# Optimization experiments

Hardware: AMD Instinct MI355X
Metric: run time of the kernel (lower is better)

The kernel has to match this reference:

```python
import jax, jax.numpy as jnp
import numpy as np
import math

N_EMBD = 2048
NUM_SLOTS = 32

def setup_inputs() -> dict:
    key = jax.random.key(0)
    ks = jax.random.split(key, 6)
    B, S, D = 4, 4096, N_EMBD
    x = jax.random.normal(ks[0], (B, S, D), dtype=jnp.float32)
    memory = jax.random.normal(ks[1], (1, NUM_SLOTS, D), dtype=jnp.float32)
    # nn.Linear weights stored as [out, in]; init scale ~ U(-1/sqrt(in), 1/sqrt(in))
    lim = 1.0 / math.sqrt(D)
    Wq = jax.random.uniform(ks[2], (D, D), minval=-lim, maxval=lim, dtype=jnp.float32)
    bq = jax.random.uniform(ks[3], (D,), minval=-lim, maxval=lim, dtype=jnp.float32)
    Wm = jax.random.uniform(ks[4], (D, D), minval=-lim, maxval=lim, dtype=jnp.float32)
    bm = jax.random.uniform(ks[5], (D,), minval=-lim, maxval=lim, dtype=jnp.float32)
    return {"x": x, "memory": memory, "Wq": Wq, "bq": bq, "Wm": Wm, "bm": bm}

def reference(x, memory, Wq, bq, Wm, bm):
    # query = x @ Wq^T + bq                         [B,S,D]
    query = jnp.einsum('bsd,ed->bse', x, Wq) + bq
    mem = memory[0]                                  # [M,D], M=32
    scale = 1.0 / math.sqrt(mem.shape[-1])
    attn = jnp.einsum('bsd,md->bsm', query, mem) * scale   # [B,S,M]
    w = jax.nn.softmax(attn, axis=-1)
    mem_out = jnp.einsum('bsm,md->bsd', w, mem)      # [B,S,D]
    mem_out = jnp.einsum('bsd,ed->bse', mem_out, Wm) + bm
    return x + mem_out
```

## Files before the change

kernel.cpp:

```cpp
#include <hip/hip_runtime.h>
#include <math.h>

#define D 2048
#define M 32
#define SCALE 0.022097086912079608f


__global__ __launch_bounds__(256) void k_wqmt(const float* __restrict__ Wq,
                                              const float* __restrict__ mem,
                                              float* __restrict__ WqmT) {
    __shared__ float memL[M * 128];
    const int t  = threadIdx.x;
    const int dc = blockIdx.x;
    const int ec = blockIdx.y;
    const int d  = dc * 256 + t;
    {
        const float4* mg = (const float4*)mem;
        float4* ml = (float4*)memL;
#pragma unroll
        for (int q = 0; q < 4; ++q) {
            int i4 = t + 256 * q;
            int m = i4 >> 5, c4 = i4 & 31;
            ml[i4] = mg[m * 512 + ec * 32 + c4];
        }
    }
    __syncthreads();
    float acc[M];
#pragma unroll
    for (int m = 0; m < M; ++m) acc[m] = 0.f;
    const float4* ml4 = (const float4*)memL;
    for (int ee = 0; ee < 128; ee += 4) {
        float q0 = Wq[(ec * 128 + ee + 0) * D + d];
        float q1 = Wq[(ec * 128 + ee + 1) * D + d];
        float q2 = Wq[(ec * 128 + ee + 2) * D + d];
        float q3 = Wq[(ec * 128 + ee + 3) * D + d];
#pragma unroll
        for (int m = 0; m < M; ++m) {
            float4 mv = ml4[m * 32 + (ee >> 2)];
            acc[m] = fmaf(q0, mv.x, fmaf(q1, mv.y, fmaf(q2, mv.z, fmaf(q3, mv.w, acc[m]))));
        }
    }
#pragma unroll
    for (int m = 0; m < M; ++m) atomicAdd(&WqmT[m * D + d], acc[m] * SCALE);
}

__global__ __launch_bounds__(256) void k_wm2(const float* __restrict__ Wm,
                                             const float* __restrict__ mem,
                                             float* __restrict__ Wm2) {
    __shared__ float tile[64 * 65];
    __shared__ float memL[M * 64];
    const int t  = threadIdx.x;
    const int et = blockIdx.x;
    const int dq = blockIdx.y;
    const int e0 = et * 64;
    const int el = t & 63, mg = t >> 6;
    float acc[8];
#pragma unroll
    for (int j = 0; j < 8; ++j) acc[j] = 0.f;
    for (int ds = 0; ds < 8; ++ds) {
        const int d0 = dq * 512 + ds * 64;
#pragma unroll
        for (int q = 0; q < 4; ++q) {
            int i  = (t >> 4) + 16 * q;
            int c4 = t & 15;
            float4 v = *(const float4*)&Wm[(e0 + i) * D + d0 + 4 * c4];
            tile[i * 65 + 4 * c4 + 0] = v.x;
            tile[i * 65 + 4 * c4 + 1] = v.y;
            tile[i * 65 + 4 * c4 + 2] = v.z;
            tile[i * 65 + 4 * c4 + 3] = v.w;
        }
#pragma unroll
        for (int q = 0; q < 2; ++q) {
            int i4 = t + 256 * q;
            int m = i4 >> 4, c4 = i4 & 15;
            *(float4*)&memL[m * 64 + 4 * c4] = *(const float4*)&mem[m * D + d0 + 4 * c4];
        }
        __syncthreads();
        const float4* ml4 = (const float4*)memL;
        for (int dd = 0; dd < 64; dd += 4) {
            float t0 = tile[el * 65 + dd + 0];
            float t1 = tile[el * 65 + dd + 1];
            float t2 = tile[el * 65 + dd + 2];
            float t3 = tile[el * 65 + dd + 3];
#pragma unroll
            for (int j = 0; j < 8; ++j) {
                float4 mv = ml4[(mg * 8 + j) * 16 + (dd >> 2)];
                acc[j] = fmaf(t0, mv.x, fmaf(t1, mv.y, fmaf(t2, mv.z, fmaf(t3, mv.w, acc[j]))));
            }
        }
        __syncthreads();
    }
#pragma unroll
    for (int j = 0; j < 8; ++j) atomicAdd(&Wm2[(mg * 8 + j) * D + e0 + el], acc[j]);
}

__global__ __launch_bounds__(256) void k_cq(const float* __restrict__ bq,
                                            const float* __restrict__ mem,
                                            float* __restrict__ cqs) {
    __shared__ float red[256 * 32];
    const int t = threadIdx.x;
    float acc[M];
#pragma unroll
    for (int m = 0; m < M; ++m) acc[m] = 0.f;
    for (int e = t; e < D; e += 256) {
        float b = bq[e];
#pragma unroll
        for (int m = 0; m < M; ++m) acc[m] = fmaf(b, mem[m * D + e], acc[m]);
    }
#pragma unroll
    for (int m = 0; m < M; ++m) red[t * 32 + m] = acc[m];
    __syncthreads();
    if (t < 32) {
        float s = 0.f;
        for (int i = 0; i < 256; ++i) s += red[i * 32 + t];
        cqs[t] = s * SCALE;
    }
}

__global__ __launch_bounds__(256, 2) void k_main(const float* __restrict__ x,
                                                 const float* __restrict__ WqmT,
                                                 const float* __restrict__ Wm2,
                                                 const float* __restrict__ cqs,
                                                 const float* __restrict__ bm,
                                                 float* __restrict__ out) {
    __shared__ float4 ldsW[M * 64];
    const int t    = threadIdx.x;
    const int wv   = t >> 6;
    const int lane = t & 63;
    const long row0 = (long)blockIdx.x * 8 + wv * 2;
    const float4* x40 = (const float4*)(x + row0 * D);
    const float4* x41 = (const float4*)(x + (row0 + 1) * D);
    float4 xr0[8], xr1[8];
#pragma unroll
    for (int j = 0; j < 8; ++j) { xr0[j] = x40[lane + 64 * j]; xr1[j] = x41[lane + 64 * j]; }

    float acc0[M], acc1[M];
#pragma unroll
    for (int m = 0; m < M; ++m) { acc0[m] = 0.f; acc1[m] = 0.f; }

    const float4* Wg = (const float4*)WqmT;
#pragma unroll
    for (int c = 0; c < 8; ++c) {
        {
            const int m = t >> 3, b4 = t & 7;
#pragma unroll
            for (int i = 0; i < 8; ++i)
                ldsW[m * 64 + b4 + 8 * i] = Wg[m * 512 + c * 64 + b4 + 8 * i];
        }
        __syncthreads();
        const float4 xa = xr0[c], xb = xr1[c];
#pragma unroll
        for (int m = 0; m < M; ++m) {
            float4 v = ldsW[m * 64 + lane];
            acc0[m] = fmaf(xa.x, v.x, fmaf(xa.y, v.y, fmaf(xa.z, v.z, fmaf(xa.w, v.w, acc0[m]))));
            acc1[m] = fmaf(xb.x, v.x, fmaf(xb.y, v.y, fmaf(xb.z, v.z, fmaf(xb.w, v.w, acc1[m]))));
        }
        __syncthreads();
    }

    float at0 = 0.f, at1 = 0.f;
#pragma unroll
    for (int m = 0; m < M; ++m) {
        float a0 = acc0[m], a1 = acc1[m];
#pragma unroll
        for (int s = 1; s < 64; s <<= 1) {
            a0 += __shfl_xor(a0, s, 64);
            a1 += __shfl_xor(a1, s, 64);
        }
        if ((lane & 31) == m) { at0 = a0; at1 = a1; }
    }
    const float cq = cqs[lane & 31];
    at0 += cq; at1 += cq;

    float mx0 = at0, mx1 = at1;
#pragma unroll
    for (int s = 1; s < 32; s <<= 1) {
        mx0 = fmaxf(mx0, __shfl_xor(mx0, s, 32));
        mx1 = fmaxf(mx1, __shfl_xor(mx1, s, 32));
    }
    float e0 = expf(at0 - mx0), e1 = expf(at1 - mx1);
    float s0 = e0, s1 = e1;
#pragma unroll
    for (int s = 1; s < 32; s <<= 1) {
        s0 += __shfl_xor(s0, s, 32);
        s1 += __shfl_xor(s1, s, 32);
    }
    const float w0 = e0 / s0, w1 = e1 / s1;

    const float4* W2g  = (const float4*)Wm2;
    const float4* bm4p = (const float4*)bm;
    float* o0p = out + row0 * D;
    float* o1p = out + (row0 + 1) * D;
#pragma unroll
    for (int c = 0; c < 8; ++c) {
        {
            const int m = t >> 3, b4 = t & 7;
#pragma unroll
            for (int i = 0; i < 8; ++i)
                ldsW[m * 64 + b4 + 8 * i] = W2g[m * 512 + c * 64 + b4 + 8 * i];
        }
        __syncthreads();
        float4 bmv = bm4p[lane + 64 * c];
        float4 o0 = xr0[c], o1 = xr1[c];
        o0.x += bmv.x; o0.y += bmv.y; o0.z += bmv.z; o0.w += bmv.w;
        o1.x += bmv.x; o1.y += bmv.y; o1.z += bmv.z; o1.w += bmv.w;
#pragma unroll
        for (int m = 0; m < M; ++m) {
            float wm0 = __shfl(w0, m, 32);
            float wm1 = __shfl(w1, m, 32);
            float4 v = ldsW[m * 64 + lane];
            o0.x = fmaf(wm0, v.x, o0.x); o0.y = fmaf(wm0, v.y, o0.y);
            o0.z = fmaf(wm0, v.z, o0.z); o0.w = fmaf(wm0, v.w, o0.w);
            o1.x = fmaf(wm1, v.x, o1.x); o1.y = fmaf(wm1, v.y, o1.y);
            o1.z = fmaf(wm1, v.z, o1.z); o1.w = fmaf(wm1, v.w, o1.w);
        }
        *(float4*)(o0p + 4 * lane + 256 * c) = o0;
        *(float4*)(o1p + 4 * lane + 256 * c) = o1;
        __syncthreads();
    }
}

extern "C" void kernel_launch(void* const* d_in, const int* in_sizes, int n_in,
                              void* d_out, int out_size, void* d_ws, size_t ws_size,
                              hipStream_t stream) {
    const float* x   = (const float*)d_in[0];
    const float* mem = (const float*)d_in[1];
    const float* Wq  = (const float*)d_in[2];
    const float* bq  = (const float*)d_in[3];
    const float* Wm  = (const float*)d_in[4];
    const float* bm  = (const float*)d_in[5];
    float* out = (float*)d_out;

    const size_t need = (size_t)(2 * M * D + M) * sizeof(float);
    if (ws_size < need) return;

    float* WqmT = (float*)d_ws;
    float* Wm2  = WqmT + M * D;
    float* cq   = Wm2 + M * D;

    hipMemsetAsync(d_ws, 0, (size_t)(2 * M * D) * sizeof(float), stream);

    k_wqmt<<<dim3(8, 16), 256, 0, stream>>>(Wq, mem, WqmT);
    k_wm2 <<<dim3(32, 4), 256, 0, stream>>>(Wm, mem, Wm2);
    k_cq  <<<1, 256, 0, stream>>>(bq, mem, cq);

    k_main<<<2048, 256, 0, stream>>>(x, WqmT, Wm2, cq, bm, out);
}
```

Baseline: 458.0 us.

## Merge precompute kernels and restructure main kernel around LDS-staged x rows

Replaces the three precompute kernels with a single k_pre launch. Part of its blocks computes Wq·mem with float2 loads and atomics, and the rest computes Wm·mem and the bias term per row using shuffle-tree reductions, so Wm2 no longer needs atomics or a memset. The main kernel now uses 512 threads to stage 8 rows of x into LDS via global_load_lds. Each wave handles 4 memory slots across all 8 rows, reading WqmT directly from global instead of restaging it through LDS with syncs. The output phase reads Wm2 directly from global, trading fewer barriers and launches for a larger LDS footprint (64KB) that may limit occupancy.

```diff
diff --git a/kernel.cpp b/kernel.cpp
--- a/kernel.cpp
+++ b/kernel.cpp
@@ -2,222 +2,201 @@
 #include <math.h>
 
 #define D 2048
+#define D4 512
 #define M 32
+#define ROWS 8
 #define SCALE 0.022097086912079608f
 
 
-__global__ __launch_bounds__(256) void k_wqmt(const float* __restrict__ Wq,
-                                              const float* __restrict__ mem,
-                                              float* __restrict__ WqmT) {
-    __shared__ float memL[M * 128];
-    const int t  = threadIdx.x;
-    const int dc = blockIdx.x;
-    const int ec = blockIdx.y;
-    const int d  = dc * 256 + t;
-    {
-        const float4* mg = (const float4*)mem;
-        float4* ml = (float4*)memL;
-#pragma unroll
-        for (int q = 0; q < 4; ++q) {
-            int i4 = t + 256 * q;
-            int m = i4 >> 5, c4 = i4 & 31;
-            ml[i4] = mg[m * 512 + ec * 32 + c4];
-        }
-    }
-    __syncthreads();
-    float acc[M];
-#pragma unroll
-    for (int m = 0; m < M; ++m) acc[m] = 0.f;
-    const float4* ml4 = (const float4*)memL;
-    for (int ee = 0; ee < 128; ee += 4) {
-        float q0 = Wq[(ec * 128 + ee + 0) * D + d];
-        float q1 = Wq[(ec * 128 + ee + 1) * D + d];
-        float q2 = Wq[(ec * 128 + ee + 2) * D + d];
-        float q3 = Wq[(ec * 128 + ee + 3) * D + d];
+#define GLOAD_LDS16(g, l) __builtin_amdgcn_global_load_lds( \
+    (const __attribute__((address_space(1))) void*)(g),     \
+    (__attribute__((address_space(3))) void*)(l), 16, 0, 0)
+
+__global__ __launch_bounds__(256) void k_pre(const float* __restrict__ Wq,
+                                             const float* __restrict__ Wm,
+                                             const float* __restrict__ mem,
+                                             const float* __restrict__ bq,
+                                             float* __restrict__ WqmT,
+                                             float* __restrict__ Wm2,
+                                             float* __restrict__ cqs) {
+    __shared__ float memL[M * 256];
+    const int t = threadIdx.x;
+    const int w = t >> 6, lane = t & 63;
+
+    if (blockIdx.x < 64) {
+        const int unit = blockIdx.x * 4 + w;
+        const int dc = unit & 15;
+        const int es = unit >> 4;
+        const int dl = dc * 64 + lane;
+        const float2* Wq2 = (const float2*)Wq;
+        float2 acc[M];
+#pragma unroll
+        for (int m = 0; m < M; ++m) acc[m] = make_float2(0.f, 0.f);
+        const int e0 = es * 128;
+        for (int e = e0; e < e0 + 128; ++e) {
+            float2 wv = Wq2[(size_t)e * (D / 2) + dl];
+#pragma unroll
+            for (int m = 0; m < M; ++m) {
+                float s = mem[m * D + e];
+                acc[m].x = fmaf(s, wv.x, acc[m].x);
+                acc[m].y = fmaf(s, wv.y, acc[m].y);
+            }
+        }
 #pragma unroll
         for (int m = 0; m < M; ++m) {
-            float4 mv = ml4[m * 32 + (ee >> 2)];
-            acc[m] = fmaf(q0, mv.x, fmaf(q1, mv.y, fmaf(q2, mv.z, fmaf(q3, mv.w, acc[m]))));
-        }
-    }
-#pragma unroll
-    for (int m = 0; m < M; ++m) atomicAdd(&WqmT[m * D + d], acc[m] * SCALE);
+            atomicAdd(&WqmT[m * D + 2 * dl],     acc[m].x * SCALE);
+            atomicAdd(&WqmT[m * D + 2 * dl + 1], acc[m].y * SCALE);
+        }
+    } else {
+        const int e = (blockIdx.x - 64) * 4 + w;
+        const bool active = (e < D + 1);
+        const float4* W4 = (const float4*)((e < D) ? (Wm + (size_t)e * D) : bq);
+        const float4* mem4 = (const float4*)mem;
+        float a[M];
+#pragma unroll
+        for (int m = 0; m < M; ++m) a[m] = 0.f;
+        for (int c = 0; c < 8; ++c) {
+#pragma unroll
+            for (int q = 0; q < 8; ++q) {
+                int i4 = t + 256 * q;
+                int m = i4 >> 6, k = i4 & 63;
+                ((float4*)memL)[i4] = mem4[m * D4 + c * 64 + k];
+            }
+            __syncthreads();
+            if (active) {
+                float4 wr = W4[c * 64 + lane];
+#pragma unroll
+                for (int m = 0; m < M; ++m) {
+                    float4 mv = ((const float4*)memL)[m * 64 + lane];
+                    a[m] = fmaf(wr.x, mv.x, fmaf(wr.y, mv.y,
+                           fmaf(wr.z, mv.z, fmaf(wr.w, mv.w, a[m]))));
+                }
+            }
+            __syncthreads();
+        }
+#pragma unroll
+        for (int s = 0; s < 5; ++s) {
+            const int msk = 1 << s;
+            const int bit = (lane >> s) & 1;
+            const int n = 32 >> s;
+#pragma unroll
+            for (int i = 0; i < n / 2; ++i) {
+                float send = bit ? a[2 * i] : a[2 * i + 1];
+                float recv = __shfl_xor(send, msk, 64);
+                a[i] = (bit ? a[2 * i + 1] : a[2 * i]) + recv;
+            }
+        }
+        float tot = a[0] + __shfl_xor(a[0], 32, 64);
+        if (active && lane < 32) {
+            if (e < D) Wm2[lane * D + e] = tot;
+            else       cqs[lane] = tot * SCALE;
+        }
+    }
 }
 
-__global__ __launch_bounds__(256) void k_wm2(const float* __restrict__ Wm,
-                                             const float* __restrict__ mem,
-                                             float* __restrict__ Wm2) {
-    __shared__ float tile[64 * 65];
-    __shared__ float memL[M * 64];
-    const int t  = threadIdx.x;
-    const int et = blockIdx.x;
-    const int dq = blockIdx.y;
-    const int e0 = et * 64;
-    const int el = t & 63, mg = t >> 6;
-    float acc[8];
-#pragma unroll
-    for (int j = 0; j < 8; ++j) acc[j] = 0.f;
-    for (int ds = 0; ds < 8; ++ds) {
-        const int d0 = dq * 512 + ds * 64;
-#pragma unroll
-        for (int q = 0; q < 4; ++q) {
-            int i  = (t >> 4) + 16 * q;
-            int c4 = t & 15;
-            float4 v = *(const float4*)&Wm[(e0 + i) * D + d0 + 4 * c4];
-            tile[i * 65 + 4 * c4 + 0] = v.x;
-            tile[i * 65 + 4 * c4 + 1] = v.y;
-            tile[i * 65 + 4 * c4 + 2] = v.z;
-            tile[i * 65 + 4 * c4 + 3] = v.w;
-        }
-#pragma unroll
-        for (int q = 0; q < 2; ++q) {
-            int i4 = t + 256 * q;
-            int m = i4 >> 4, c4 = i4 & 15;
-            *(float4*)&memL[m * 64 + 4 * c4] = *(const float4*)&mem[m * D + d0 + 4 * c4];
-        }
-        __syncthreads();
-        const float4* ml4 = (const float4*)memL;
-        for (int dd = 0; dd < 64; dd += 4) {
-            float t0 = tile[el * 65 + dd + 0];
-            float t1 = tile[el * 65 + dd + 1];
-            float t2 = tile[el * 65 + dd + 2];
-            float t3 = tile[el * 65 + dd + 3];
-#pragma unroll
-            for (int j = 0; j < 8; ++j) {
-                float4 mv = ml4[(mg * 8 + j) * 16 + (dd >> 2)];
-                acc[j] = fmaf(t0, mv.x, fmaf(t1, mv.y, fmaf(t2, mv.z, fmaf(t3, mv.w, acc[j]))));
-            }
-        }
-        __syncthreads();
-    }
-#pragma unroll
-    for (int j = 0; j < 8; ++j) atomicAdd(&Wm2[(mg * 8 + j) * D + e0 + el], acc[j]);
-}
-
-__global__ __launch_bounds__(256) void k_cq(const float* __restrict__ bq,
-                                            const float* __restrict__ mem,
-                                            float* __restrict__ cqs) {
-    __shared__ float red[256 * 32];
-    const int t = threadIdx.x;
-    float acc[M];
-#pragma unroll
-    for (int m = 0; m < M; ++m) acc[m] = 0.f;
-    for (int e = t; e < D; e += 256) {
-        float b = bq[e];
-#pragma unroll
-        for (int m = 0; m < M; ++m) acc[m] = fmaf(b, mem[m * D + e], acc[m]);
-    }
-#pragma unroll
-    for (int m = 0; m < M; ++m) red[t * 32 + m] = acc[m];
-    __syncthreads();
-    if (t < 32) {
-        float s = 0.f;
-        for (int i = 0; i < 256; ++i) s += red[i * 32 + t];
-        cqs[t] = s * SCALE;
-    }
-}
-
-__global__ __launch_bounds__(256, 2) void k_main(const float* __restrict__ x,
+__global__ __launch_bounds__(512, 2) void k_main(const float* __restrict__ x,
                                                  const float* __restrict__ WqmT,
                                                  const float* __restrict__ Wm2,
                                                  const float* __restrict__ cqs,
                                                  const float* __restrict__ bm,
                                                  float* __restrict__ out) {
-    __shared__ float4 ldsW[M * 64];
-    const int t    = threadIdx.x;
-    const int wv   = t >> 6;
-    const int lane = t & 63;
-    const long row0 = (long)blockIdx.x * 8 + wv * 2;
-    const float4* x40 = (const float4*)(x + row0 * D);
-    const float4* x41 = (const float4*)(x + (row0 + 1) * D);
-    float4 xr0[8], xr1[8];
-#pragma unroll
-    for (int j = 0; j < 8; ++j) { xr0[j] = x40[lane + 64 * j]; xr1[j] = x41[lane + 64 * j]; }
-
-    float acc0[M], acc1[M];
-#pragma unroll
-    for (int m = 0; m < M; ++m) { acc0[m] = 0.f; acc1[m] = 0.f; }
-
-    const float4* Wg = (const float4*)WqmT;
+    __shared__ float xs[ROWS * D];
+    __shared__ float attnL[ROWS * M];
+    __shared__ float4 wT[M * 2];
+    const int t = threadIdx.x;
+    const int w = t >> 6, lane = t & 63;
+    const long row0 = (long)blockIdx.x * ROWS;
+    const float* xg = x + row0 * D;
+
+#pragma unroll
+    for (int i = 0; i < 8; ++i) {
+        const int off = w * 2048 + i * 256;
+        GLOAD_LDS16(xg + off + lane * 4, xs + off);
+    }
+
+    float a[M];
+#pragma unroll
+    for (int i = 0; i < M; ++i) a[i] = 0.f;
+    const float4* xs4 = (const float4*)xs;
+    const float4* Wg4 = (const float4*)WqmT + (size_t)(4 * w) * D4;
+
+    __syncthreads();
+
 #pragma unroll
     for (int c = 0; c < 8; ++c) {
-        {
-            const int m = t >> 3, b4 = t & 7;
-#pragma unroll
-            for (int i = 0; i < 8; ++i)
-                ldsW[m * 64 + b4 + 8 * i] = Wg[m * 512 + c * 64 + b4 + 8 * i];
-        }
-        __syncthreads();
-        const float4 xa = xr0[c], xb = xr1[c];
-#pragma unroll
-        for (int m = 0; m < M; ++m) {
-            float4 v = ldsW[m * 64 + lane];
-            acc0[m] = fmaf(xa.x, v.x, fmaf(xa.y, v.y, fmaf(xa.z, v.z, fmaf(xa.w, v.w, acc0[m]))));
-            acc1[m] = fmaf(xb.x, v.x, fmaf(xb.y, v.y, fmaf(xb.z, v.z, fmaf(xb.w, v.w, acc1[m]))));
-        }
-        __syncthreads();
-    }
-
-    float at0 = 0.f, at1 = 0.f;
+        float4 wq[4];
+#pragma unroll
+        for (int j = 0; j < 4; ++j) wq[j] = Wg4[j * D4 + c * 64 + lane];
+#pragma unroll
+        for (int r = 0; r < ROWS; ++r) {
+            float4 xv = xs4[r * D4 + c * 64 + lane];
+#pragma unroll
+            for (int j = 0; j < 4; ++j) {
+                a[j * 8 + r] = fmaf(wq[j].x, xv.x, fmaf(wq[j].y, xv.y,
+                               fmaf(wq[j].z, xv.z, fmaf(wq[j].w, xv.w, a[j * 8 + r]))));
+            }
+        }
+    }
+#pragma unroll
+    for (int s = 0; s < 5; ++s) {
+        const int msk = 1 << s;
+        const int bit = (lane >> s) & 1;
+        const int n = 32 >> s;
+#pragma unroll
+        for (int i = 0; i < n / 2; ++i) {
+            float send = bit ? a[2 * i] : a[2 * i + 1];
+            float recv = __shfl_xor(send, msk, 64);
+            a[i] = (bit ? a[2 * i + 1] : a[2 * i]) + recv;
+        }
+    }
+    float tot = a[0] + __shfl_xor(a[0], 32, 64);
+    {
+        const int j = (lane >> 3) & 3, r = lane & 7;
+        const int m = 4 * w + j;
+        if (lane < 32) attnL[r * M + m] = tot + cqs[m];
+    }
+    __syncthreads();
+
+    if (t < 256) {
+        const int r = t >> 5, m = t & 31;
+        float v = attnL[r * M + m];
+        float mx = v;
+#pragma unroll
+        for (int s2 = 1; s2 < 32; s2 <<= 1) mx = fmaxf(mx, __shfl_xor(mx, s2, 32));
+        float e = expf(v - mx);
+        float sum = e;
+#pragma unroll
+        for (int s2 = 1; s2 < 32; s2 <<= 1) sum += __shfl_xor(sum, s2, 32);
+        ((float*)wT)[m * ROWS + r] = e / sum;
+    }
+    __syncthreads();
+
+    const int base = w * 64 + lane;
+    const float4* W2 = (const float4*)Wm2;
+    const float4 bv = ((const float4*)bm)[base];
+    float4 o[ROWS];
+#pragma unroll
+    for (int r = 0; r < ROWS; ++r) {
+        float4 xv = xs4[r * D4 + base];
+        o[r] = make_float4(xv.x + bv.x, xv.y + bv.y, xv.z + bv.z, xv.w + bv.w);
+    }
 #pragma unroll
     for (int m = 0; m < M; ++m) {
-        float a0 = acc0[m], a1 = acc1[m];
-#pragma unroll
-        for (int s = 1; s < 64; s <<= 1) {
-            a0 += __shfl_xor(a0, s, 64);
-            a1 += __shfl_xor(a1, s, 64);
-        }
-        if ((lane & 31) == m) { at0 = a0; at1 = a1; }
-    }
-    const float cq = cqs[lane & 31];
-    at0 += cq; at1 += cq;
-
-    float mx0 = at0, mx1 = at1;
-#pragma unroll
-    for (int s = 1; s < 32; s <<= 1) {
-        mx0 = fmaxf(mx0, __shfl_xor(mx0, s, 32));
-        mx1 = fmaxf(mx1, __shfl_xor(mx1, s, 32));
-    }
-    float e0 = expf(at0 - mx0), e1 = expf(at1 - mx1);
-    float s0 = e0, s1 = e1;
-#pragma unroll
-    for (int s = 1; s < 32; s <<= 1) {
-        s0 += __shfl_xor(s0, s, 32);
-        s1 += __shfl_xor(s1, s, 32);
-    }
-    const float w0 = e0 / s0, w1 = e1 / s1;
-
-    const float4* W2g  = (const float4*)Wm2;
-    const float4* bm4p = (const float4*)bm;
-    float* o0p = out + row0 * D;
-    float* o1p = out + (row0 + 1) * D;
-#pragma unroll
-    for (int c = 0; c < 8; ++c) {
-        {
-            const int m = t >> 3, b4 = t & 7;
-#pragma unroll
-            for (int i = 0; i < 8; ++i)
-                ldsW[m * 64 + b4 + 8 * i] = W2g[m * 512 + c * 64 + b4 + 8 * i];
-        }
-        __syncthreads();
-        float4 bmv = bm4p[lane + 64 * c];
-        float4 o0 = xr0[c], o1 = xr1[c];
-        o0.x += bmv.x; o0.y += bmv.y; o0.z += bmv.z; o0.w += bmv.w;
-        o1.x += bmv.x; o1.y += bmv.y; o1.z += bmv.z; o1.w += bmv.w;
-#pragma unroll
-        for (int m = 0; m < M; ++m) {
-            float wm0 = __shfl(w0, m, 32);
-            float wm1 = __shfl(w1, m, 32);
-            float4 v = ldsW[m * 64 + lane];
-            o0.x = fmaf(wm0, v.x, o0.x); o0.y = fmaf(wm0, v.y, o0.y);
-            o0.z = fmaf(wm0, v.z, o0.z); o0.w = fmaf(wm0, v.w, o0.w);
-            o1.x = fmaf(wm1, v.x, o1.x); o1.y = fmaf(wm1, v.y, o1.y);
-            o1.z = fmaf(wm1, v.z, o1.z); o1.w = fmaf(wm1, v.w, o1.w);
-        }
-        *(float4*)(o0p + 4 * lane + 256 * c) = o0;
-        *(float4*)(o1p + 4 * lane + 256 * c) = o1;
-        __syncthreads();
-    }
+        float4 wv = W2[(size_t)m * D4 + base];
+        float4 wa = wT[m * 2];
+        float4 wb = wT[m * 2 + 1];
+        const float wr[8] = {wa.x, wa.y, wa.z, wa.w, wb.x, wb.y, wb.z, wb.w};
+#pragma unroll
+        for (int r = 0; r < ROWS; ++r) {
+            o[r].x = fmaf(wr[r], wv.x, o[r].x);
+            o[r].y = fmaf(wr[r], wv.y, o[r].y);
+            o[r].z = fmaf(wr[r], wv.z, o[r].z);
+            o[r].w = fmaf(wr[r], wv.w, o[r].w);
+        }
+    }
+    float4* og = (float4*)(out + row0 * D);
+#pragma unroll
+    for (int r = 0; r < ROWS; ++r) og[r * D4 + base] = o[r];
 }
 
 extern "C" void kernel_launch(void* const* d_in, const int* in_sizes, int n_in,
@@ -238,11 +217,8 @@
     float* Wm2  = WqmT + M * D;
     float* cq   = Wm2 + M * D;
 
-    hipMemsetAsync(d_ws, 0, (size_t)(2 * M * D) * sizeof(float), stream);
-
-    k_wqmt<<<dim3(8, 16), 256, 0, stream>>>(Wq, mem, WqmT);
-    k_wm2 <<<dim3(32, 4), 256, 0, stream>>>(Wm, mem, Wm2);
-    k_cq  <<<1, 256, 0, stream>>>(bq, mem, cq);
-
-    k_main<<<2048, 256, 0, stream>>>(x, WqmT, Wm2, cq, bm, out);
+    hipMemsetAsync(WqmT, 0, (size_t)(M * D) * sizeof(float), stream);
+
+    k_pre <<<64 + 513, 256, 0, stream>>>(Wq, Wm, mem, bq, WqmT, Wm2, cq);
+    k_main<<<2048, 512, 0, stream>>>(x, WqmT, Wm2, cq, bm, out);
 }
```

Result: slower. 473.6 us (+3.4%).
